# Performance work log

Measured on AMD Instinct MI355X. Metric: run time of the kernel, lower is better.

The kernel has to match this reference:

```python
import jax, jax.numpy as jnp
import numpy as np

D, P, S, E = 200, 200, 150, 150  # drugs, proteins, diseases, side-effects
EMB = 256

def setup_inputs() -> dict:
    key = jax.random.key(0)
    ks = jax.random.split(key, 10)
    s = 0.05
    type_mask = jnp.concatenate([
        jnp.zeros(D, jnp.int64) if False else jnp.full((D,), 0, jnp.int32),
        jnp.full((P,), 1, jnp.int32),
        jnp.full((S,), 2, jnp.int32),
        jnp.full((E,), 3, jnp.int32)]).astype(jnp.int32)
    return {
        'type_mask': type_mask,
        'entity_embedding': jax.random.normal(ks[0], (D + P + S + E, EMB)) * s,
        'relation_embedding': jax.random.normal(ks[1], (1200, EMB)) * s,
        'W_ent': jax.random.normal(ks[2], (EMB, EMB)) * s,
        'W_rel': jax.random.normal(ks[3], (EMB, EMB)) * s,
        'W1': jax.random.normal(ks[4], (2 * EMB, 1024)) * s,
        'b1': jnp.zeros((1024,)),
        'W2': jax.random.normal(ks[5], (1024, 512)) * s,
        'b2': jnp.zeros((512,)),
        'W3': jax.random.normal(ks[6], (512, 2)) * s,
        'b3': jnp.zeros((2,)),
    }

def _pair_softmax(a, b, W1, b1, W2, b2, W3, b3):
    # classifier(concat(a[i], b[j])) for the full cartesian product.
    # First linear is decomposed: W1 @ [a;b] = a@W1a + b@W1b (same math,
    # avoids materializing the [Na*Nb, 2*EMB] concat tensor).
    W1a, W1b = W1[:EMB], W1[EMB:]
    ha = a @ W1a                      # [Na, 1024]
    hb = b @ W1b                      # [Nb, 1024]
    h = jax.nn.relu(ha[:, None, :] + hb[None, :, :] + b1)  # [Na, Nb, 1024]
    h = jax.nn.relu(h @ W2 + b2)      # [Na, Nb, 512]
    logits = h @ W3 + b3              # [Na, Nb, 2]
    Na, Nb = a.shape[0], b.shape[0]
    return jax.nn.softmax(logits.reshape(Na * Nb, 2), axis=-1)

def reference(type_mask, entity_embedding, relation_embedding, W_ent, W_rel,
              W1, b1, W2, b2, W3, b3):
    tm = np.asarray(type_mask)  # concrete, block-structured type ids
    idx = [np.nonzero(tm == t)[0] for t in range(4)]
    # project embeddings (project_on path; nn.Linear: x @ W)
    ent = entity_embedding @ W_ent
    _rel = relation_embedding @ W_rel  # computed in original forward, unused (graph_on off)
    drug, prot, dis, se = (ent[idx[0]], ent[idx[1]], ent[idx[2]], ent[idx[3]])
    cls = lambda a, b: _pair_softmax(a, b, W1, b1, W2, b2, W3, b3)
    out_dp = cls(drug, prot)
    out_dd = cls(drug, drug)
    out_ds = cls(drug, dis)
    out_de = cls(drug, se)
    out_ps = cls(prot, dis)
    out_pp = cls(prot, prot)
    out_pd = cls(prot, drug)
    out_ed = cls(se, drug)
    out_sp = cls(dis, prot)
    out_sd = cls(dis, drug)
    return (out_dp, out_dd, out_ds, out_de, out_ps, out_pp, out_pd,
            out_ed, out_sp, out_sd, drug)
```

## Files before the change

kernel.cpp:

```cpp
#include <hip/hip_runtime.h>
#include <hip/hip_bf16.h>

typedef __attribute__((ext_vector_type(4))) float floatx4;
typedef __attribute__((ext_vector_type(8))) __bf16 bf16x8;
typedef unsigned short ushort_t;

#define NENT  700
#define EMB   256
#define KDIM  1024
#define NDIM  512
#define HROWS 720
#define NPAIR 340000

#define WS_HA   0
#define WS_HB   (WS_HA + HROWS*KDIM*2)
#define WS_W2H  (WS_HB + HROWS*KDIM*2)
#define WS_ENT  (WS_W2H + NDIM*KDIM*2)
#define WS_LG   (WS_ENT + NENT*EMB*4)

__device__ __forceinline__ float ldin(const void* p, int i, int isbf) {
    return isbf ? __bfloat162float(((const __hip_bfloat16*)p)[i])
                : ((const float*)p)[i];
}

__device__ __forceinline__ int detect_bf16(const ushort_t* __restrict__ w) {
    int t = threadIdx.x & 63;
    int e = (w[2*t] >> 7) & 0xFF;
    unsigned long long m = __ballot(e >= 100 && e <= 126);
    return (__popcll(m) >= 48) ? 1 : 0;
}

#define LDS_BARRIER() do { __builtin_amdgcn_s_waitcnt(0xC07F); __builtin_amdgcn_s_barrier(); } while (0)

__global__ void entprep_kernel(const void* __restrict__ E, const void* __restrict__ Went,
                               const void* __restrict__ W2,
                               float* __restrict__ ent, __hip_bfloat16* __restrict__ W2H,
                               void* __restrict__ out) {
    int isbf = detect_bf16((const ushort_t*)E);
    if (blockIdx.x < 88) {
        int ib = blockIdx.x * 8, t = threadIdx.x;
        __shared__ float rows[8][EMB];
#pragma unroll
        for (int r = 0; r < 8; ++r) {
            int i = ib + r;
            rows[r][t] = (i < NENT) ? ldin(E, i*EMB + t, isbf) : 0.f;
        }
        __syncthreads();
        float acc[8] = {0.f,0.f,0.f,0.f,0.f,0.f,0.f,0.f};
        if (isbf) {
            const __hip_bfloat16* W = (const __hip_bfloat16*)Went;
            for (int k = 0; k < EMB; ++k) {
                float w = __bfloat162float(W[k*EMB + t]);
#pragma unroll
                for (int r = 0; r < 8; ++r) acc[r] += rows[r][k] * w;
            }
        } else {
            const float* W = (const float*)Went;
            for (int k = 0; k < EMB; ++k) {
                float w = W[k*EMB + t];
#pragma unroll
                for (int r = 0; r < 8; ++r) acc[r] += rows[r][k] * w;
            }
        }
#pragma unroll
        for (int r = 0; r < 8; ++r) {
            int i = ib + r;
            if (i < NENT) {
                ent[i*EMB + t] = acc[r];
                if (i < 200) {
                    if (isbf) ((__hip_bfloat16*)out)[680000 + i*EMB + t] = __float2bfloat16(acc[r]);
                    else      ((float*)out)[680000 + i*EMB + t] = acc[r];
                }
            }
        }
    } else {
        int g = (blockIdx.x - 88)*256 + threadIdx.x;
        int lane = g & 63, f = (g >> 6) & 15, kc = (g >> 10) & 31, half = g >> 15;
        int l15 = lane & 15, quad = lane >> 4;
        int n = half*256 + f*16 + l15;
        bf16x8 v;
#pragma unroll
        for (int j = 0; j < 8; ++j) {
            int k = kc*32 + quad*8 + j;
            v[j] = (__bf16)ldin(W2, k*NDIM + n, isbf);
        }
        *(bf16x8*)(W2H + (size_t)g*8) = v;
    }
}

__global__ void hab_kernel(const float* __restrict__ ent, const void* __restrict__ E,
                           const void* __restrict__ W1, const void* __restrict__ b1,
                           __hip_bfloat16* __restrict__ HA, __hip_bfloat16* __restrict__ HB) {
    int isbf = detect_bf16((const ushort_t*)E);
    int part = blockIdx.y;
    int ib = blockIdx.x * 16;
    int t = threadIdx.x;
    __shared__ float rows[16][EMB];
#pragma unroll
    for (int r = 0; r < 16; ++r) {
        int i = ib + r;
        rows[r][t] = (i < NENT) ? ent[i*EMB + t] : 0.f;
    }
    __syncthreads();
    float acc[16][4];
#pragma unroll
    for (int r = 0; r < 16; ++r)
#pragma unroll
        for (int p = 0; p < 4; ++p) acc[r][p] = 0.f;

    int wbase = part*EMB*KDIM;
    if (isbf) {
        const __hip_bfloat16* W = (const __hip_bfloat16*)W1;
        for (int k = 0; k < EMB; ++k) {
            float w[4];
#pragma unroll
            for (int p = 0; p < 4; ++p) w[p] = __bfloat162float(W[wbase + k*KDIM + t + p*256]);
#pragma unroll
            for (int r = 0; r < 16; ++r) {
                float e = rows[r][k];
#pragma unroll
                for (int p = 0; p < 4; ++p) acc[r][p] += e * w[p];
            }
        }
    } else {
        const float* W = (const float*)W1;
        for (int k = 0; k < EMB; ++k) {
            float w[4];
#pragma unroll
            for (int p = 0; p < 4; ++p) w[p] = W[wbase + k*KDIM + t + p*256];
#pragma unroll
            for (int r = 0; r < 16; ++r) {
                float e = rows[r][k];
#pragma unroll
                for (int p = 0; p < 4; ++p) acc[r][p] += e * w[p];
            }
        }
    }
    __hip_bfloat16* HX = part ? HB : HA;
#pragma unroll
    for (int r = 0; r < 16; ++r) {
#pragma unroll
        for (int p = 0; p < 4; ++p) {
            int n = t + p*256;
            float v = acc[r][p];
            if (!part) v += ldin(b1, n, isbf);
            HX[(ib + r)*KDIM + n] = __float2bfloat16(v);
        }
    }
}

union U8 { bf16x8 v; unsigned u[4]; };

__device__ __forceinline__ bf16x8 mk_af3(bf16x8 ha, bf16x8 hb) {
    U8 r;
#pragma unroll
    for (int j = 0; j < 4; ++j) {
        float x0 = fmaxf((float)ha[2*j]   + (float)hb[2*j],   0.f);
        float x1 = fmaxf((float)ha[2*j+1] + (float)hb[2*j+1], 0.f);
        unsigned u0 = __float_as_uint(x0) + 0x8000u;
        unsigned u1 = __float_as_uint(x1) + 0x8000u;
#if defined(__has_builtin) && __has_builtin(__builtin_amdgcn_perm)
        r.u[j] = __builtin_amdgcn_perm(u1, u0, 0x07060302u);
#else
        r.u[j] = (u0 >> 16) | (u1 & 0xFFFF0000u);
#endif
    }
    return r.v;
}

#define MFMA(a, b, c) __builtin_amdgcn_mfma_f32_16x16x32_bf16((a), (b), (c), 0, 0, 0)

__global__ __launch_bounds__(256, 3) void pair_kernel(
        const ushort_t* __restrict__ HA, const ushort_t* __restrict__ HB,
        const ushort_t* __restrict__ W2H, const void* __restrict__ E,
        const void* __restrict__ b2, const void* __restrict__ W3,
        float* __restrict__ Lg, void* __restrict__ out) {

    const int blkEnd[10] = {650,1300,1800,2300,2800,3450,4100,4594,5088,5582};
    const int aB[10]  = {0,0,0,0,200,200,200,550,400,400};
    const int bB[10]  = {200,0,400,550,400,200,0,0,200,0};
    const int NaT[10] = {200,200,200,200,200,200,200,150,150,150};
    const int NbT[10] = {200,200,150,150,150,200,200,200,200,200};
    const int jTl[10] = {13,13,10,10,10,13,13,13,13,13};
    const int oOf[10] = {0,80000,160000,220000,280000,340000,420000,500000,560000,620000};

    __shared__ __align__(16) unsigned char sAF[16384];
    __shared__ float lgt[4][64][2];

    int bid = blockIdx.x;
    int half = blockIdx.y;
    int ty = 0;
    while (bid >= blkEnd[ty]) ty++;
    int lb = bid - (ty ? blkEnd[ty-1] : 0);
    int jT = jTl[ty];
    int it = lb / jT;
    int jt = lb - it*jT;
    int i0 = aB[ty] + it*4;
    int j0 = bB[ty] + jt*16;

    int tid  = threadIdx.x;
    int lane = tid & 63;
    int w    = tid >> 6;
    int l15  = lane & 15;
    int quad = lane >> 4;
    int kb   = (bid*7 + half*3) & 31;

    const char* WB = (const char*)W2H + ((size_t)((half*32)*16 + w*4))*1024 + lane*16;
    const ushort_t* HBp = HB + (j0 + l15)*KDIM + quad*8;
    const ushort_t* HAp = HA + (i0 + w)*KDIM + quad*8;

    floatx4 acc[4][4];
#pragma unroll
    for (int mf = 0; mf < 4; ++mf)
#pragma unroll
        for (int nf = 0; nf < 4; ++nf) acc[mf][nf] = (floatx4){0.f,0.f,0.f,0.f};

    int k0 = kb, k1 = (kb + 1) & 31;
    bf16x8 Bc0 = *(const bf16x8*)(WB + (size_t)k0*16384);
    bf16x8 Bc1 = *(const bf16x8*)(WB + (size_t)k0*16384 + 1024);
    bf16x8 Bc2 = *(const bf16x8*)(WB + (size_t)k0*16384 + 2048);
    bf16x8 Bc3 = *(const bf16x8*)(WB + (size_t)k0*16384 + 3072);
    bf16x8 Bn0 = *(const bf16x8*)(WB + (size_t)k1*16384);
    bf16x8 Bn1 = *(const bf16x8*)(WB + (size_t)k1*16384 + 1024);
    bf16x8 Bn2 = *(const bf16x8*)(WB + (size_t)k1*16384 + 2048);
    bf16x8 Bn3 = *(const bf16x8*)(WB + (size_t)k1*16384 + 3072);
    bf16x8 haA = *(const bf16x8*)(HAp + k0*32);
    bf16x8 haB = *(const bf16x8*)(HAp + k1*32);
    bf16x8 hbA = *(const bf16x8*)(HBp + k0*32);
    bf16x8 hbB = *(const bf16x8*)(HBp + k1*32);

#pragma unroll 2
    for (int ph = 0; ph < 16; ++ph) {
        int kn2 = (2*ph + 2 + kb) & 31;
        int kn3 = (2*ph + 3 + kb) & 31;
        bf16x8 nhaA = *(const bf16x8*)(HAp + kn2*32);
        bf16x8 nhaB = *(const bf16x8*)(HAp + kn3*32);
        bf16x8 nhbA = *(const bf16x8*)(HBp + kn2*32);
        bf16x8 nhbB = *(const bf16x8*)(HBp + kn3*32);

        char* sW = (char*)sAF + (ph & 1)*8192 + w*1024 + lane*16;
        *(bf16x8*)(sW)        = mk_af3(haA, hbA);
        *(bf16x8*)(sW + 4096) = mk_af3(haB, hbB);
        LDS_BARRIER();

        const char* sR = (const char*)sAF + (ph & 1)*8192 + lane*16;
        {
            bf16x8 a0 = *(const bf16x8*)(sR);
            bf16x8 a1 = *(const bf16x8*)(sR + 1024);
            bf16x8 a2 = *(const bf16x8*)(sR + 2048);
            bf16x8 a3 = *(const bf16x8*)(sR + 3072);
            acc[0][0] = MFMA(a0, Bc0, acc[0][0]); acc[1][0] = MFMA(a1, Bc0, acc[1][0]);
            acc[2][0] = MFMA(a2, Bc0, acc[2][0]); acc[3][0] = MFMA(a3, Bc0, acc[3][0]);
            acc[0][1] = MFMA(a0, Bc1, acc[0][1]); acc[1][1] = MFMA(a1, Bc1, acc[1][1]);
            acc[2][1] = MFMA(a2, Bc1, acc[2][1]); acc[3][1] = MFMA(a3, Bc1, acc[3][1]);
            acc[0][2] = MFMA(a0, Bc2, acc[0][2]); acc[1][2] = MFMA(a1, Bc2, acc[1][2]);
            acc[2][2] = MFMA(a2, Bc2, acc[2][2]); acc[3][2] = MFMA(a3, Bc2, acc[3][2]);
            acc[0][3] = MFMA(a0, Bc3, acc[0][3]); acc[1][3] = MFMA(a1, Bc3, acc[1][3]);
            acc[2][3] = MFMA(a2, Bc3, acc[2][3]); acc[3][3] = MFMA(a3, Bc3, acc[3][3]);
        }
        Bc0 = *(const bf16x8*)(WB + (size_t)kn2*16384);
        Bc1 = *(const bf16x8*)(WB + (size_t)kn2*16384 + 1024);
        Bc2 = *(const bf16x8*)(WB + (size_t)kn2*16384 + 2048);
        Bc3 = *(const bf16x8*)(WB + (size_t)kn2*16384 + 3072);
        {
            bf16x8 a0 = *(const bf16x8*)(sR + 4096);
            bf16x8 a1 = *(const bf16x8*)(sR + 4096 + 1024);
            bf16x8 a2 = *(const bf16x8*)(sR + 4096 + 2048);
            bf16x8 a3 = *(const bf16x8*)(sR + 4096 + 3072);
            acc[0][0] = MFMA(a0, Bn0, acc[0][0]); acc[1][0] = MFMA(a1, Bn0, acc[1][0]);
            acc[2][0] = MFMA(a2, Bn0, acc[2][0]); acc[3][0] = MFMA(a3, Bn0, acc[3][0]);
            acc[0][1] = MFMA(a0, Bn1, acc[0][1]); acc[1][1] = MFMA(a1, Bn1, acc[1][1]);
            acc[2][1] = MFMA(a2, Bn1, acc[2][1]); acc[3][1] = MFMA(a3, Bn1, acc[3][1]);
            acc[0][2] = MFMA(a0, Bn2, acc[0][2]); acc[1][2] = MFMA(a1, Bn2, acc[1][2]);
            acc[2][2] = MFMA(a2, Bn2, acc[2][2]); acc[3][2] = MFMA(a3, Bn2, acc[3][2]);
            acc[0][3] = MFMA(a0, Bn3, acc[0][3]); acc[1][3] = MFMA(a1, Bn3, acc[1][3]);
            acc[2][3] = MFMA(a2, Bn3, acc[2][3]); acc[3][3] = MFMA(a3, Bn3, acc[3][3]);
        }
        Bn0 = *(const bf16x8*)(WB + (size_t)kn3*16384);
        Bn1 = *(const bf16x8*)(WB + (size_t)kn3*16384 + 1024);
        Bn2 = *(const bf16x8*)(WB + (size_t)kn3*16384 + 2048);
        Bn3 = *(const bf16x8*)(WB + (size_t)kn3*16384 + 3072);

        haA = nhaA; haB = nhaB; hbA = nhbA; hbB = nhbB;
    }

    int isbf = detect_bf16((const ushort_t*)E);
    int nb = half*256 + w*64;
    float b2v[4], wa[4], wb[4];
#pragma unroll
    for (int nf = 0; nf < 4; ++nf) {
        int n = nb + nf*16 + l15;
        b2v[nf] = ldin(b2, n, isbf);
        wa[nf]  = ldin(W3, 2*n, isbf);
        wb[nf]  = ldin(W3, 2*n+1, isbf);
    }
#pragma unroll
    for (int mf = 0; mf < 4; ++mf) {
        float s0[4] = {0.f,0.f,0.f,0.f};
        float s1[4] = {0.f,0.f,0.f,0.f};
#pragma unroll
        for (int nf = 0; nf < 4; ++nf) {
            floatx4 c = acc[mf][nf];
#pragma unroll
            for (int r = 0; r < 4; ++r) {
                float v = fmaxf(c[r] + b2v[nf], 0.f);
                s0[r] += v * wa[nf];
                s1[r] += v * wb[nf];
            }
        }
#pragma unroll
        for (int off = 1; off < 16; off <<= 1) {
#pragma unroll
            for (int r = 0; r < 4; ++r) {
                s0[r] += __shfl_xor(s0[r], off, 64);
                s1[r] += __shfl_xor(s1[r], off, 64);
            }
        }
        if (l15 == 0) {
#pragma unroll
            for (int r = 0; r < 4; ++r) {
                int p = mf*16 + quad*4 + r;
                lgt[w][p][0] = s0[r];
                lgt[w][p][1] = s1[r];
            }
        }
    }
    __syncthreads();

    if (tid < 64) {
        int p = tid;
        float l0 = lgt[0][p][0] + lgt[1][p][0] + lgt[2][p][0] + lgt[3][p][0];
        float l1 = lgt[0][p][1] + lgt[1][p][1] + lgt[2][p][1] + lgt[3][p][1];
        int pi = it*4 + (p >> 4), pj = jt*16 + (p & 15);
        if (pi < NaT[ty] && pj < NbT[ty]) {
            int o = oOf[ty] + (pi*NbT[ty] + pj)*2;
            if (half == 0) {
                if (isbf) {
                    __hip_bfloat16* ob = (__hip_bfloat16*)out;
                    ob[o] = __float2bfloat16(l0); ob[o+1] = __float2bfloat16(l1);
                } else {
                    float* of = (float*)out;
                    of[o] = l0; of[o+1] = l1;
                }
            } else {
                Lg[o] = l0; Lg[o+1] = l1;
            }
        }
    }
}

__global__ void final_kernel(const float* __restrict__ Lg, const void* __restrict__ b3,
                             const void* __restrict__ E, void* __restrict__ out) {
    int isbf = detect_bf16((const ushort_t*)E);
    int g = blockIdx.x*512 + threadIdx.x;
    if (g >= NPAIR) return;
    float h0, h1;
    if (isbf) {
        h0 = __bfloat162float(((const __hip_bfloat16*)out)[2*g]);
        h1 = __bfloat162float(((const __hip_bfloat16*)out)[2*g+1]);
    } else {
        h0 = ((const float*)out)[2*g];
        h1 = ((const float*)out)[2*g+1];
    }
    float l0 = h0 + Lg[2*g]   + ldin(b3, 0, isbf);
    float l1 = h1 + Lg[2*g+1] + ldin(b3, 1, isbf);
    float mx = fmaxf(l0, l1);
    float e0 = __expf(l0 - mx), e1 = __expf(l1 - mx);
    float inv = 1.f / (e0 + e1);
    if (isbf) {
        __hip_bfloat16* ob = (__hip_bfloat16*)out;
        ob[2*g]   = __float2bfloat16(e0 * inv);
        ob[2*g+1] = __float2bfloat16(e1 * inv);
    } else {
        float* of = (float*)out;
        of[2*g]   = e0 * inv;
        of[2*g+1] = e1 * inv;
    }
}

extern "C" void kernel_launch(void* const* d_in, const int* in_sizes, int n_in,
                              void* d_out, int out_size, void* d_ws, size_t ws_size,
                              hipStream_t stream) {
    const void* E    = d_in[1];
    const void* Went = d_in[3];
    const void* W1   = d_in[5];
    const void* b1   = d_in[6];
    const void* W2   = d_in[7];
    const void* b2   = d_in[8];
    const void* W3   = d_in[9];
    const void* b3   = d_in[10];

    char* ws = (char*)d_ws;
    __hip_bfloat16* HA   = (__hip_bfloat16*)(ws + WS_HA);
    __hip_bfloat16* HB   = (__hip_bfloat16*)(ws + WS_HB);
    __hip_bfloat16* W2H  = (__hip_bfloat16*)(ws + WS_W2H);
    float*          entf = (float*)(ws + WS_ENT);
    float*          Lg   = (float*)(ws + WS_LG);

    entprep_kernel<<<dim3(344), dim3(256), 0, stream>>>(E, Went, W2, entf, W2H, d_out);
    hab_kernel<<<dim3(45, 2), dim3(256), 0, stream>>>(entf, E, W1, b1, HA, HB);
    pair_kernel<<<dim3(5582, 2), dim3(256), 0, stream>>>((const ushort_t*)HA, (const ushort_t*)HB,
                                                         (const ushort_t*)W2H, E, b2, W3, Lg, d_out);
    final_kernel<<<dim3((NPAIR + 511)/512), dim3(512), 0, stream>>>(Lg, b3, E, d_out);
}
```

Measured before the change: 563.2 us.

## Merge N-halves into one 512-thread block and fuse softmax into pair kernel

The two blockIdx.y halves of the W2 output dimension become one 512-thread block. Waves 0-3 and 4-7 each cover one 256-column half and also split the A-fragment construction (ReLU(ha+hb)) between them, so each pair tile is built once instead of twice. All eight waves' partial logits are reduced in shared memory, then b3 and the 2-way softmax are applied in place. This removes the separate final kernel and the Lg partial-logit round trip through global memory. In exchange, each block uses more registers and threads, and occupancy moves from 3 blocks of 256 to 2 blocks of 512 per CU.

```diff
diff --git a/kernel.cpp b/kernel.cpp
--- a/kernel.cpp
+++ b/kernel.cpp
@@ -170,11 +170,11 @@
 
 #define MFMA(a, b, c) __builtin_amdgcn_mfma_f32_16x16x32_bf16((a), (b), (c), 0, 0, 0)
 
-__global__ __launch_bounds__(256, 3) void pair_kernel(
+__global__ __launch_bounds__(512, 2) void pair_kernel(
         const ushort_t* __restrict__ HA, const ushort_t* __restrict__ HB,
         const ushort_t* __restrict__ W2H, const void* __restrict__ E,
         const void* __restrict__ b2, const void* __restrict__ W3,
-        float* __restrict__ Lg, void* __restrict__ out) {
+        const void* __restrict__ b3, void* __restrict__ out) {
 
     const int blkEnd[10] = {650,1300,1800,2300,2800,3450,4100,4594,5088,5582};
     const int aB[10]  = {0,0,0,0,200,200,200,550,400,400};
@@ -185,10 +185,9 @@
     const int oOf[10] = {0,80000,160000,220000,280000,340000,420000,500000,560000,620000};
 
     __shared__ __align__(16) unsigned char sAF[16384];
-    __shared__ float lgt[4][64][2];
+    __shared__ float lgt[8][64][2];
 
     int bid = blockIdx.x;
-    int half = blockIdx.y;
     int ty = 0;
     while (bid >= blkEnd[ty]) ty++;
     int lb = bid - (ty ? blkEnd[ty-1] : 0);
@@ -201,13 +200,15 @@
     int tid  = threadIdx.x;
     int lane = tid & 63;
     int w    = tid >> 6;
+    int w3_  = w & 3;
+    int wh   = w >> 2;
     int l15  = lane & 15;
     int quad = lane >> 4;
-    int kb   = (bid*7 + half*3) & 31;
-
-    const char* WB = (const char*)W2H + ((size_t)((half*32)*16 + w*4))*1024 + lane*16;
+    int kb   = (bid*7) & 31;
+
+    const char* WB = (const char*)W2H + ((size_t)(wh*512 + w3_*4))*1024 + lane*16;
     const ushort_t* HBp = HB + (j0 + l15)*KDIM + quad*8;
-    const ushort_t* HAp = HA + (i0 + w)*KDIM + quad*8;
+    const ushort_t* HAp = HA + (i0 + w3_)*KDIM + quad*8;
 
     floatx4 acc[4][4];
 #pragma unroll
@@ -224,26 +225,23 @@
     bf16x8 Bn1 = *(const bf16x8*)(WB + (size_t)k1*16384 + 1024);
     bf16x8 Bn2 = *(const bf16x8*)(WB + (size_t)k1*16384 + 2048);
     bf16x8 Bn3 = *(const bf16x8*)(WB + (size_t)k1*16384 + 3072);
-    bf16x8 haA = *(const bf16x8*)(HAp + k0*32);
-    bf16x8 haB = *(const bf16x8*)(HAp + k1*32);
-    bf16x8 hbA = *(const bf16x8*)(HBp + k0*32);
-    bf16x8 hbB = *(const bf16x8*)(HBp + k1*32);
+
+    int kg0 = (kb + wh) & 31;
+    bf16x8 ha = *(const bf16x8*)(HAp + kg0*32);
+    bf16x8 hb = *(const bf16x8*)(HBp + kg0*32);
 
 #pragma unroll 2
     for (int ph = 0; ph < 16; ++ph) {
-        int kn2 = (2*ph + 2 + kb) & 31;
-        int kn3 = (2*ph + 3 + kb) & 31;
-        bf16x8 nhaA = *(const bf16x8*)(HAp + kn2*32);
-        bf16x8 nhaB = *(const bf16x8*)(HAp + kn3*32);
-        bf16x8 nhbA = *(const bf16x8*)(HBp + kn2*32);
-        bf16x8 nhbB = *(const bf16x8*)(HBp + kn3*32);
-
         char* sW = (char*)sAF + (ph & 1)*8192 + w*1024 + lane*16;
-        *(bf16x8*)(sW)        = mk_af3(haA, hbA);
-        *(bf16x8*)(sW + 4096) = mk_af3(haB, hbB);
+        *(bf16x8*)sW = mk_af3(ha, hb);
+        int kgn = (kb + 2*(ph + 1) + wh) & 31;
+        ha = *(const bf16x8*)(HAp + kgn*32);
+        hb = *(const bf16x8*)(HBp + kgn*32);
         LDS_BARRIER();
 
         const char* sR = (const char*)sAF + (ph & 1)*8192 + lane*16;
+        int kn2 = (kb + 2*ph + 2) & 31;
+        int kn3 = (kb + 2*ph + 3) & 31;
         {
             bf16x8 a0 = *(const bf16x8*)(sR);
             bf16x8 a1 = *(const bf16x8*)(sR + 1024);
@@ -280,12 +278,10 @@
         Bn1 = *(const bf16x8*)(WB + (size_t)kn3*16384 + 1024);
         Bn2 = *(const bf16x8*)(WB + (size_t)kn3*16384 + 2048);
         Bn3 = *(const bf16x8*)(WB + (size_t)kn3*16384 + 3072);
-
-        haA = nhaA; haB = nhaB; hbA = nhbA; hbB = nhbB;
     }
 
     int isbf = detect_bf16((const ushort_t*)E);
-    int nb = half*256 + w*64;
+    int nb = wh*256 + w3_*64;
     float b2v[4], wa[4], wb[4];
 #pragma unroll
     for (int nf = 0; nf < 4; ++nf) {
@@ -329,52 +325,27 @@
 
     if (tid < 64) {
         int p = tid;
-        float l0 = lgt[0][p][0] + lgt[1][p][0] + lgt[2][p][0] + lgt[3][p][0];
-        float l1 = lgt[0][p][1] + lgt[1][p][1] + lgt[2][p][1] + lgt[3][p][1];
+        float l0 = 0.f, l1 = 0.f;
+#pragma unroll
+        for (int ww = 0; ww < 8; ++ww) { l0 += lgt[ww][p][0]; l1 += lgt[ww][p][1]; }
+        l0 += ldin(b3, 0, isbf);
+        l1 += ldin(b3, 1, isbf);
         int pi = it*4 + (p >> 4), pj = jt*16 + (p & 15);
         if (pi < NaT[ty] && pj < NbT[ty]) {
+            float mx = fmaxf(l0, l1);
+            float e0 = __expf(l0 - mx), e1 = __expf(l1 - mx);
+            float inv = 1.f / (e0 + e1);
             int o = oOf[ty] + (pi*NbT[ty] + pj)*2;
-            if (half == 0) {
-                if (isbf) {
-                    __hip_bfloat16* ob = (__hip_bfloat16*)out;
-                    ob[o] = __float2bfloat16(l0); ob[o+1] = __float2bfloat16(l1);
-                } else {
-                    float* of = (float*)out;
-                    of[o] = l0; of[o+1] = l1;
-                }
+            if (isbf) {
+                __hip_bfloat16* ob = (__hip_bfloat16*)out;
+                ob[o]   = __float2bfloat16(e0 * inv);
+                ob[o+1] = __float2bfloat16(e1 * inv);
             } else {
-                Lg[o] = l0; Lg[o+1] = l1;
-            }
-        }
-    }
-}
-
-__global__ void final_kernel(const float* __restrict__ Lg, const void* __restrict__ b3,
-                             const void* __restrict__ E, void* __restrict__ out) {
-    int isbf = detect_bf16((const ushort_t*)E);
-    int g = blockIdx.x*512 + threadIdx.x;
-    if (g >= NPAIR) return;
-    float h0, h1;
-    if (isbf) {
-        h0 = __bfloat162float(((const __hip_bfloat16*)out)[2*g]);
-        h1 = __bfloat162float(((const __hip_bfloat16*)out)[2*g+1]);
-    } else {
-        h0 = ((const float*)out)[2*g];
-        h1 = ((const float*)out)[2*g+1];
-    }
-    float l0 = h0 + Lg[2*g]   + ldin(b3, 0, isbf);
-    float l1 = h1 + Lg[2*g+1] + ldin(b3, 1, isbf);
-    float mx = fmaxf(l0, l1);
-    float e0 = __expf(l0 - mx), e1 = __expf(l1 - mx);
-    float inv = 1.f / (e0 + e1);
-    if (isbf) {
-        __hip_bfloat16* ob = (__hip_bfloat16*)out;
-        ob[2*g]   = __float2bfloat16(e0 * inv);
-        ob[2*g+1] = __float2bfloat16(e1 * inv);
-    } else {
-        float* of = (float*)out;
-        of[2*g]   = e0 * inv;
-        of[2*g+1] = e1 * inv;
+                float* of = (float*)out;
+                of[o]   = e0 * inv;
+                of[o+1] = e1 * inv;
+            }
+        }
     }
 }
 
@@ -395,11 +366,9 @@
     __hip_bfloat16* HB   = (__hip_bfloat16*)(ws + WS_HB);
     __hip_bfloat16* W2H  = (__hip_bfloat16*)(ws + WS_W2H);
     float*          entf = (float*)(ws + WS_ENT);
-    float*          Lg   = (float*)(ws + WS_LG);
 
     entprep_kernel<<<dim3(344), dim3(256), 0, stream>>>(E, Went, W2, entf, W2H, d_out);
     hab_kernel<<<dim3(45, 2), dim3(256), 0, stream>>>(entf, E, W1, b1, HA, HB);
-    pair_kernel<<<dim3(5582, 2), dim3(256), 0, stream>>>((const ushort_t*)HA, (const ushort_t*)HB,
-                                                         (const ushort_t*)W2H, E, b2, W3, Lg, d_out);
-    final_kernel<<<dim3((NPAIR + 511)/512), dim3(512), 0, stream>>>(Lg, b3, E, d_out);
-}
+    pair_kernel<<<dim3(5582), dim3(512), 0, stream>>>((const ushort_t*)HA, (const ushort_t*)HB,
+                                                      (const ushort_t*)W2H, E, b2, W3, b3, d_out);
+}
```

Result: no change. 562.8 us (-0.1%).
